# Performance work log

Measured on AMD Instinct MI355X. Metric: run time of the kernel, lower is better.

Reference implementation:

```python
import jax, jax.numpy as jnp
import numpy as np

TEMPERATURE = 0.5
EPS = 1e-8          # torch CosineSimilarity denominator clamp
NEG_INF = -1e30     # finite stand-in for -inf padding (grad-safe)


def setup_inputs() -> dict:
    key = jax.random.key(0)
    k1, k2, k3 = jax.random.split(key, 3)
    B, D = 4096, 256
    z_i = jax.random.normal(k1, (B, D), dtype=jnp.float32)
    z_j = jax.random.normal(k2, (B, D), dtype=jnp.float32)
    labels = jax.random.randint(k3, (B,), 0, 100, dtype=jnp.int64)
    return {"z_i": z_i, "z_j": z_j, "labels": labels}


def reference(z_i, z_j, labels):
    B = z_i.shape[0]
    z = jnp.concatenate([z_i, z_j], axis=0)          # [N, D], N = 2B
    lab = jnp.concatenate([labels, labels], axis=0)  # [N]
    N = 2 * B

    # cosine similarity matrix / temperature
    norm = jnp.maximum(jnp.linalg.norm(z, axis=1, keepdims=True), EPS)
    zn = z / norm                                    # [N, D]
    sim = (zn @ zn.T) / TEMPERATURE                  # [N, N]

    # positives: sim[i, i+B] and sim[i+B, i]
    pos = jnp.concatenate(
        [jnp.diagonal(sim, offset=B), jnp.diagonal(sim, offset=-B)], axis=0
    )                                                # [N]

    # negatives mask: different label (diagonal & positive pair share a label,
    # so torch's explicit zeroing of them is already implied by label inequality)
    mask = lab[:, None] != lab[None, :]              # [N, N] bool

    # CE with target index 0 over [pos | padded negatives]:
    # loss_i = logsumexp(pos_i, negs_i) - pos_i  (padding -inf is a no-op in lse)
    neg_logits = jnp.where(mask, sim, NEG_INF)       # [N, N]
    row_max = jnp.maximum(pos, jnp.max(neg_logits, axis=1))          # [N]
    lse = row_max + jnp.log(
        jnp.exp(pos - row_max)
        + jnp.sum(jnp.exp(neg_logits - row_max[:, None]), axis=1)
    )                                                # [N]
    loss = jnp.sum(lse - pos) / N
    return loss
```

## Files before the change

kernel.cpp:

```cpp
#include <hip/hip_runtime.h>
#include <hip/hip_bf16.h>


#define B_ 4096
#define N_ 8192
#define D_ 256
#define EPS_ 1e-8f
#define SPLITS 16
#define BM 128
#define BN 64
#define KC 8
#define CPS (N_ / SPLITS)
#define NT_ (CPS / BN)
#define LOG2E 1.44269504088896340736f

typedef __attribute__((ext_vector_type(8))) short bfrag_t;
typedef __attribute__((ext_vector_type(4))) float f32x4_t;

__device__ __forceinline__ ushort f2bf_rne(float x) {
  union { float f; unsigned u; } a; a.f = x;
  unsigned r = a.u + 0x7FFFu + ((a.u >> 16) & 1u);
  return (ushort)(r >> 16);
}

__device__ __forceinline__ void cp16_lds(const uint4* g, uint4* l) {
  __builtin_amdgcn_global_load_lds(
      (const __attribute__((address_space(1))) unsigned int*)g,
      (__attribute__((address_space(3))) unsigned int*)l, 16, 0, 0);
}

__global__ __launch_bounds__(256) void k_prep(
    const float* __restrict__ zi, const float* __restrict__ zj,
    ushort* __restrict__ zn, float* __restrict__ pos) {
  const int w = threadIdx.x >> 6, lane = threadIdx.x & 63;
  const int p = blockIdx.x * 4 + w;
  float4 a = reinterpret_cast<const float4*>(zi + (size_t)p * D_)[lane];
  float4 b = reinterpret_cast<const float4*>(zj + (size_t)p * D_)[lane];
  float si = a.x * a.x + a.y * a.y + a.z * a.z + a.w * a.w;
  float sj = b.x * b.x + b.y * b.y + b.z * b.z + b.w * b.w;
  float dd = a.x * b.x + a.y * b.y + a.z * b.z + a.w * b.w;
#pragma unroll
  for (int d = 1; d < 64; d <<= 1) {
    si += __shfl_xor(si, d);
    sj += __shfl_xor(sj, d);
    dd += __shfl_xor(dd, d);
  }
  const float ni = fmaxf(sqrtf(si), EPS_), nj = fmaxf(sqrtf(sj), EPS_);
  const float ii = 1.0f / ni, ij = 1.0f / nj;
  ushort4 oi, oj;
  oi.x = f2bf_rne(a.x * ii); oi.y = f2bf_rne(a.y * ii);
  oi.z = f2bf_rne(a.z * ii); oi.w = f2bf_rne(a.w * ii);
  oj.x = f2bf_rne(b.x * ij); oj.y = f2bf_rne(b.y * ij);
  oj.z = f2bf_rne(b.z * ij); oj.w = f2bf_rne(b.w * ij);
  reinterpret_cast<ushort4*>(zn + (size_t)p * D_)[lane] = oi;
  reinterpret_cast<ushort4*>(zn + (size_t)(p + B_) * D_)[lane] = oj;
  if (lane == 0) {
    float v = dd / (ni * nj) * 2.0f;
    pos[p] = v;
    pos[p + B_] = v;
  }
}

__global__ __launch_bounds__(256) void k_flash(
    const ushort* __restrict__ zn, const int* __restrict__ labels,
    float* __restrict__ Spart) {
  __shared__ uint4 lds16[BN * 32];
  const int tid = threadIdx.x;
  const int w = tid >> 6, lane = tid & 63;
  const int l15 = lane & 15, l4 = lane >> 4;
  const int c31 = lane & 31, lh = lane >> 5;
  const int arowb = blockIdx.x * BM + w * 32;
  const int split = blockIdx.y;

  bfrag_t a[2][KC];
#pragma unroll
  for (int mf = 0; mf < 2; ++mf) {
    const int ar = arowb + mf * 16 + l15;
#pragma unroll
    for (int kc = 0; kc < KC; ++kc)
      a[mf][kc] = *reinterpret_cast<const bfrag_t*>(
          zn + (size_t)ar * D_ + kc * 32 + l4 * 8);
  }

  int labR[2][4];
#pragma unroll
  for (int mf = 0; mf < 2; ++mf)
#pragma unroll
    for (int rg = 0; rg < 4; ++rg)
      labR[mf][rg] = labels[(arowb + mf * 16 + l4 * 4 + rg) & (B_ - 1)];

  float Srun[2][4];
#pragma unroll
  for (int mf = 0; mf < 2; ++mf)
#pragma unroll
    for (int rg = 0; rg < 4; ++rg) Srun[mf][rg] = 0.f;

  const uint4* g16 = reinterpret_cast<const uint4*>(zn);

  auto stage = [&](int ct) {
    const int cb = split * CPS + ct * BN;
    const uint4* gt = g16 + (size_t)cb * 32;
#pragma unroll
    for (int q = 0; q < 8; ++q) {
      const int rw = w * 16 + q * 2 + lh;
      const int src = rw * 32 + (c31 ^ (rw & 7));
      cp16_lds(gt + src, lds16 + (w * 512 + q * 64));
    }
  };

  stage(0);

  for (int ct = 0; ct < NT_; ++ct) {
    const int cb = split * CPS + ct * BN;
    __syncthreads();

    int labC[4];
#pragma unroll
    for (int nf = 0; nf < 4; ++nf)
      labC[nf] = labels[(cb + nf * 16 + l15) & (B_ - 1)];

    f32x4_t acc[2][4];
#pragma unroll
    for (int mf = 0; mf < 2; ++mf)
#pragma unroll
      for (int nf = 0; nf < 4; ++nf)
        acc[mf][nf] = (f32x4_t){0.f, 0.f, 0.f, 0.f};

#pragma unroll
    for (int kc = 0; kc < KC; ++kc) {
#pragma unroll
      for (int nf = 0; nf < 4; ++nf) {
        const int br = nf * 16 + l15;
        const int cu = kc * 4 + l4;
        bfrag_t bf = *reinterpret_cast<const bfrag_t*>(
            &lds16[br * 32 + (cu ^ (br & 7))]);
        acc[0][nf] = __builtin_amdgcn_mfma_f32_16x16x32_bf16(a[0][kc], bf, acc[0][nf], 0, 0, 0);
        acc[1][nf] = __builtin_amdgcn_mfma_f32_16x16x32_bf16(a[1][kc], bf, acc[1][nf], 0, 0, 0);
      }
    }

    __syncthreads();
    if (ct + 1 < NT_) stage(ct + 1);

#pragma unroll
    for (int mf = 0; mf < 2; ++mf) {
#pragma unroll
      for (int rg = 0; rg < 4; ++rg) {
        const int rl = labR[mf][rg];
        float s0 = 0.f, s1 = 0.f;
#pragma unroll
        for (int nf = 0; nf < 4; ++nf) {
          float t = fmaf(acc[mf][nf][rg], 2.0f * LOG2E, -2.0f * LOG2E);
          float e = __builtin_amdgcn_exp2f(t);
          e = (labC[nf] != rl) ? e : 0.0f;
          if (nf & 1) s1 += e; else s0 += e;
        }
        Srun[mf][rg] += s0 + s1;
      }
    }
  }

#pragma unroll
  for (int mf = 0; mf < 2; ++mf) {
#pragma unroll
    for (int rg = 0; rg < 4; ++rg) {
      float s = Srun[mf][rg];
#pragma unroll
      for (int d = 1; d < 16; d <<= 1) s += __shfl_xor(s, d);
      if (l15 == 0)
        Spart[(size_t)split * N_ + arowb + mf * 16 + l4 * 4 + rg] = s;
    }
  }
}

__global__ __launch_bounds__(256) void k_finalize(
    const float* __restrict__ Spart, const float* __restrict__ pos,
    float* __restrict__ out) {
  __shared__ float red[4];
  const int i = blockIdx.x * 256 + threadIdx.x;
  const float p = pos[i];
  float S = __builtin_amdgcn_exp2f(fmaf(p, LOG2E, -2.0f * LOG2E));
#pragma unroll
  for (int s = 0; s < SPLITS; ++s) S += Spart[s * N_ + i];
  float c = 2.0f + __logf(S) - p;
#pragma unroll
  for (int d = 1; d < 64; d <<= 1) c += __shfl_xor(c, d);
  const int w = threadIdx.x >> 6, lane = threadIdx.x & 63;
  if (lane == 0) red[w] = c;
  __syncthreads();
  if (threadIdx.x == 0) {
    float t = red[0] + red[1] + red[2] + red[3];
    atomicAdd(out, t * (1.0f / (float)N_));
  }
}

extern "C" void kernel_launch(void* const* d_in, const int* in_sizes, int n_in,
                              void* d_out, int out_size, void* d_ws, size_t ws_size,
                              hipStream_t stream) {
  (void)in_sizes; (void)n_in; (void)out_size; (void)ws_size;
  const float* zi = (const float*)d_in[0];
  const float* zj = (const float*)d_in[1];
  const int* labels = (const int*)d_in[2];
  char* ws = (char*)d_ws;
  ushort* zn   = (ushort*)(ws);
  float* pos   = (float*)(ws + 4u * 1024 * 1024);
  float* Spart = (float*)(ws + 4u * 1024 * 1024 + 32 * 1024);
  float* out = (float*)d_out;

  hipMemsetAsync(out, 0, sizeof(float), stream);
  k_prep<<<B_ / 4, 256, 0, stream>>>(zi, zj, zn, pos);
  k_flash<<<dim3(N_ / BM, SPLITS), 256, 0, stream>>>(zn, labels, Spart);
  k_finalize<<<N_ / 256, 256, 0, stream>>>(Spart, pos, out);
}
```

Baseline: 108.6 us.

## Double-buffer column tiles, cache labels in LDS, swizzle blocks, single-block finalize

The flash kernel now works on 32-column tiles held in two LDS buffers, so the async global-to-LDS copy of the next tile overlaps the MFMA and exp work on the current one, leaving one barrier per iteration. Column labels are loaded once into LDS, the 2D grid is flattened with a block-index swizzle to group blocks that share column data, and LDS addresses are precomputed. The finalize step becomes a single 1024-thread block that writes the result directly, which removes the memset and the atomic. The smaller tile halves MFMA work per barrier and the launch-bounds occupancy hint may limit registers.

```diff
diff --git a/kernel.cpp b/kernel.cpp
--- a/kernel.cpp
+++ b/kernel.cpp
@@ -8,7 +8,7 @@
 #define EPS_ 1e-8f
 #define SPLITS 16
 #define BM 128
-#define BN 64
+#define BN 32
 #define KC 8
 #define CPS (N_ / SPLITS)
 #define NT_ (CPS / BN)
@@ -61,16 +61,20 @@
   }
 }
 
-__global__ __launch_bounds__(256) void k_flash(
+__global__ __launch_bounds__(256, 4) void k_flash(
     const ushort* __restrict__ zn, const int* __restrict__ labels,
     float* __restrict__ Spart) {
-  __shared__ uint4 lds16[BN * 32];
+  __shared__ uint4 lds16[2 * BN * 32];
+  __shared__ int labbuf[CPS];
   const int tid = threadIdx.x;
   const int w = tid >> 6, lane = tid & 63;
   const int l15 = lane & 15, l4 = lane >> 4;
   const int c31 = lane & 31, lh = lane >> 5;
-  const int arowb = blockIdx.x * BM + w * 32;
-  const int split = blockIdx.y;
+
+  const int bid = blockIdx.x;
+  const int swz = (bid & 7) * 128 + (bid >> 3);
+  const int rowblk = swz & 63, split = swz >> 6;
+  const int arowb = rowblk * BM + w * 32;
 
   bfrag_t a[2][KC];
 #pragma unroll
@@ -82,6 +86,9 @@
           zn + (size_t)ar * D_ + kc * 32 + l4 * 8);
   }
 
+  labbuf[tid]       = labels[(split * CPS + tid) & (B_ - 1)];
+  labbuf[tid + 256] = labels[(split * CPS + tid + 256) & (B_ - 1)];
+
   int labR[2][4];
 #pragma unroll
   for (int mf = 0; mf < 2; ++mf)
@@ -95,69 +102,78 @@
 #pragma unroll
     for (int rg = 0; rg < 4; ++rg) Srun[mf][rg] = 0.f;
 
-  const uint4* g16 = reinterpret_cast<const uint4*>(zn);
-
-  auto stage = [&](int ct) {
-    const int cb = split * CPS + ct * BN;
-    const uint4* gt = g16 + (size_t)cb * 32;
-#pragma unroll
-    for (int q = 0; q < 8; ++q) {
-      const int rw = w * 16 + q * 2 + lh;
-      const int src = rw * 32 + (c31 ^ (rw & 7));
-      cp16_lds(gt + src, lds16 + (w * 512 + q * 64));
-    }
+  const int offp0 = l15 * 512 + ((l4 ^ (l15 & 7)) << 4);
+  const int offp1 = l15 * 512 + (((4 + l4) ^ (l15 & 7)) << 4);
+  uint so[4];
+#pragma unroll
+  for (int q = 0; q < 4; ++q) {
+    const int rw = w * 8 + q * 2 + lh;
+    so[q] = rw * 32 + (c31 ^ (rw & 7));
+  }
+  const uint4* gsplit =
+      reinterpret_cast<const uint4*>(zn) + (size_t)(split * CPS) * 32;
+
+  auto stage = [&](int t) {
+    const uint4* gt = gsplit + t * (BN * 32);
+    uint4* db = lds16 + ((t & 1) * (BN * 32)) + w * 256;
+#pragma unroll
+    for (int q = 0; q < 4; ++q) cp16_lds(gt + so[q], db + q * 64);
   };
 
   stage(0);
-
+  __syncthreads();
+
+#pragma unroll 2
   for (int ct = 0; ct < NT_; ++ct) {
-    const int cb = split * CPS + ct * BN;
-    __syncthreads();
-
-    int labC[4];
-#pragma unroll
-    for (int nf = 0; nf < 4; ++nf)
-      labC[nf] = labels[(cb + nf * 16 + l15) & (B_ - 1)];
-
-    f32x4_t acc[2][4];
+    if (ct + 1 < NT_) stage(ct + 1);
+
+    int labC[2];
+#pragma unroll
+    for (int nf = 0; nf < 2; ++nf)
+      labC[nf] = labbuf[ct * BN + nf * 16 + l15];
+
+    f32x4_t acc[2][2];
 #pragma unroll
     for (int mf = 0; mf < 2; ++mf)
 #pragma unroll
-      for (int nf = 0; nf < 4; ++nf)
+      for (int nf = 0; nf < 2; ++nf)
         acc[mf][nf] = (f32x4_t){0.f, 0.f, 0.f, 0.f};
 
+    const char* lb = (const char*)lds16 + ((ct & 1) << 14);
 #pragma unroll
     for (int kc = 0; kc < KC; ++kc) {
-#pragma unroll
-      for (int nf = 0; nf < 4; ++nf) {
-        const int br = nf * 16 + l15;
-        const int cu = kc * 4 + l4;
+      const int kimm = (kc >> 1) << 7;
+      const int po = (kc & 1) ? offp1 : offp0;
+#pragma unroll
+      for (int nf = 0; nf < 2; ++nf) {
         bfrag_t bf = *reinterpret_cast<const bfrag_t*>(
-            &lds16[br * 32 + (cu ^ (br & 7))]);
+            lb + po + nf * 8192 + kimm);
         acc[0][nf] = __builtin_amdgcn_mfma_f32_16x16x32_bf16(a[0][kc], bf, acc[0][nf], 0, 0, 0);
         acc[1][nf] = __builtin_amdgcn_mfma_f32_16x16x32_bf16(a[1][kc], bf, acc[1][nf], 0, 0, 0);
       }
     }
 
-    __syncthreads();
-    if (ct + 1 < NT_) stage(ct + 1);
-
 #pragma unroll
     for (int mf = 0; mf < 2; ++mf) {
 #pragma unroll
       for (int rg = 0; rg < 4; ++rg) {
         const int rl = labR[mf][rg];
-        float s0 = 0.f, s1 = 0.f;
-#pragma unroll
-        for (int nf = 0; nf < 4; ++nf) {
-          float t = fmaf(acc[mf][nf][rg], 2.0f * LOG2E, -2.0f * LOG2E);
-          float e = __builtin_amdgcn_exp2f(t);
-          e = (labC[nf] != rl) ? e : 0.0f;
-          if (nf & 1) s1 += e; else s0 += e;
+        float e0, e1;
+        {
+          float t0 = fmaf(acc[mf][0][rg], 2.0f * LOG2E, -2.0f * LOG2E);
+          e0 = __builtin_amdgcn_exp2f(t0);
+          e0 = (labC[0] != rl) ? e0 : 0.0f;
         }
-        Srun[mf][rg] += s0 + s1;
+        {
+          float t1 = fmaf(acc[mf][1][rg], 2.0f * LOG2E, -2.0f * LOG2E);
+          e1 = __builtin_amdgcn_exp2f(t1);
+          e1 = (labC[1] != rl) ? e1 : 0.0f;
+        }
+        Srun[mf][rg] += e0 + e1;
       }
     }
+
+    __syncthreads();
   }
 
 #pragma unroll
@@ -173,24 +189,30 @@
   }
 }
 
-__global__ __launch_bounds__(256) void k_finalize(
+__global__ __launch_bounds__(1024) void k_finalize(
     const float* __restrict__ Spart, const float* __restrict__ pos,
     float* __restrict__ out) {
-  __shared__ float red[4];
-  const int i = blockIdx.x * 256 + threadIdx.x;
-  const float p = pos[i];
-  float S = __builtin_amdgcn_exp2f(fmaf(p, LOG2E, -2.0f * LOG2E));
-#pragma unroll
-  for (int s = 0; s < SPLITS; ++s) S += Spart[s * N_ + i];
-  float c = 2.0f + __logf(S) - p;
+  __shared__ float red[16];
+  const int tid = threadIdx.x;
+  float c = 0.f;
+#pragma unroll
+  for (int k = 0; k < 8; ++k) {
+    const int i = k * 1024 + tid;
+    const float p = pos[i];
+    float S = __builtin_amdgcn_exp2f(fmaf(p, LOG2E, -2.0f * LOG2E));
+#pragma unroll
+    for (int s = 0; s < SPLITS; ++s) S += Spart[s * N_ + i];
+    c += 2.0f + __logf(S) - p;
+  }
 #pragma unroll
   for (int d = 1; d < 64; d <<= 1) c += __shfl_xor(c, d);
-  const int w = threadIdx.x >> 6, lane = threadIdx.x & 63;
-  if (lane == 0) red[w] = c;
+  if ((tid & 63) == 0) red[tid >> 6] = c;
   __syncthreads();
-  if (threadIdx.x == 0) {
-    float t = red[0] + red[1] + red[2] + red[3];
-    atomicAdd(out, t * (1.0f / (float)N_));
+  if (tid == 0) {
+    float t = 0.f;
+#pragma unroll
+    for (int q = 0; q < 16; ++q) t += red[q];
+    out[0] = t * (1.0f / (float)N_);
   }
 }
 
@@ -207,8 +229,7 @@
   float* Spart = (float*)(ws + 4u * 1024 * 1024 + 32 * 1024);
   float* out = (float*)d_out;
 
-  hipMemsetAsync(out, 0, sizeof(float), stream);
   k_prep<<<B_ / 4, 256, 0, stream>>>(zi, zj, zn, pos);
-  k_flash<<<dim3(N_ / BM, SPLITS), 256, 0, stream>>>(zn, labels, Spart);
-  k_finalize<<<N_ / 256, 256, 0, stream>>>(Spart, pos, out);
-}
+  k_flash<<<(N_ / BM) * SPLITS, 256, 0, stream>>>(zn, labels, Spart);
+  k_finalize<<<1, 1024, 0, stream>>>(Spart, pos, out);
+}
```

Measured after the change: 111.7 us. 1.03x slower.
